# Kernel optimization log

Hardware: AMD Instinct MI355X
Metric: run time of the kernel (lower is better)

Reference implementation:

```python
import jax, jax.numpy as jnp
import numpy as np

B, T, SEQ = 8, 129, 128
H, N, NL, NE, V = 512, 64, 4, 128, 18

def _gelu(x):
    return jax.nn.gelu(x, approximate=False)

def _conv2d(x, w, b, stride):
    y = jax.lax.conv_general_dilated(x, w, (stride, stride), 'VALID',
                                     dimension_numbers=('NCHW', 'OIHW', 'NCHW'))
    return y + b[None, :, None, None]

def _layernorm(x, g, b, eps=1e-5):
    mu = jnp.mean(x, axis=-1, keepdims=True)
    var = jnp.mean(jnp.square(x - mu), axis=-1, keepdims=True)
    return (x - mu) * jax.lax.rsqrt(var + eps) * g + b

def _s4_kernel(log_dt, A_re, A_im, C_re, C_im, L):
    # Diagonal SSM (ZOH discretization, B=1): K[h,l] = 2*Re(sum_n Ceff * exp(dt*A)^l)
    dt = jnp.exp(log_dt)[:, None]                  # [H,1]
    A = A_re + 1j * A_im                            # [H,N] complex64
    dtA = (dt * A).astype(jnp.complex64)
    C = (C_re + 1j * C_im).astype(jnp.complex64)
    Ceff = C * (jnp.exp(dtA) - 1.0) / A             # [H,N]
    vand = jnp.exp(dtA[:, :, None] * jnp.arange(L, dtype=jnp.float32))  # [H,N,L]
    return 2.0 * jnp.einsum('hn,hnl->hl', Ceff, vand).real

def _fft_conv(u, K, D):
    # u: [B,H,L]  K: [H,L]  causal conv via zero-padded FFT
    L = u.shape[-1]
    n = 2 * L
    Uf = jnp.fft.rfft(u, n=n)
    Kf = jnp.fft.rfft(K, n=n)
    y = jnp.fft.irfft(Uf * Kf[None], n=n)[..., :L]
    return y + D[None, :, None] * u

def setup_inputs() -> dict:
    key = jax.random.key(0)
    ks = jax.random.split(key, 32)
    d = {}
    d['states'] = jax.random.uniform(ks[0], (B, T, 4, 84, 84), dtype=jnp.float32)
    d['actions'] = jax.random.randint(ks[1], (B, T), 0, V)
    d['rtgs'] = jax.random.uniform(ks[2], (B, T, 1), dtype=jnp.float32)
    s = 0.02
    d['enc_w1'] = jax.random.normal(ks[3], (32, 4, 8, 8)) * s
    d['enc_b1'] = jnp.zeros((32,))
    d['enc_w2'] = jax.random.normal(ks[4], (64, 32, 4, 4)) * s
    d['enc_b2'] = jnp.zeros((64,))
    d['enc_w3'] = jax.random.normal(ks[5], (64, 64, 3, 3)) * s
    d['enc_b3'] = jnp.zeros((64,))
    d['enc_lw'] = jax.random.normal(ks[6], (3136, NE)) * s
    d['enc_lb'] = jnp.zeros((NE,))
    d['ret_w'] = jax.random.normal(ks[7], (1, NE)) * s
    d['ret_b'] = jnp.zeros((NE,))
    d['act_emb'] = jax.random.normal(ks[8], (V, NE)) * s
    d['proj_w'] = jax.random.normal(ks[9], (3 * NE, H)) * s
    d['proj_b'] = jnp.zeros((H,))
    d['pre_w'] = jax.random.normal(ks[10], (H, H)) * s
    d['pre_b'] = jnp.zeros((H,))
    d['ln_g'] = jnp.ones((NL, H))
    d['ln_b'] = jnp.zeros((NL, H))
    lo, hi = np.log(1e-3), np.log(1e-1)
    d['log_dt'] = lo + jax.random.uniform(ks[11], (NL, H)) * (hi - lo)
    d['A_re'] = -0.5 * jnp.ones((NL, H, N))
    d['A_im'] = jnp.broadcast_to(np.pi * jnp.arange(N, dtype=jnp.float32), (NL, H, N)).copy()
    d['C_re'] = jax.random.normal(ks[12], (NL, H, N)) * (0.5 ** 0.5)
    d['C_im'] = jax.random.normal(ks[13], (NL, H, N)) * (0.5 ** 0.5)
    d['Dp'] = jax.random.normal(ks[14], (NL, H))
    d['aft_w'] = jax.random.normal(ks[15], (NL, H, H)) * s
    d['aft_b'] = jnp.zeros((NL, H))
    d['out_w'] = jax.random.normal(ks[16], (H, V)) * s
    return d

def reference(states, actions, rtgs, enc_w1, enc_b1, enc_w2, enc_b2, enc_w3, enc_b3,
              enc_lw, enc_lb, ret_w, ret_b, act_emb, proj_w, proj_b, pre_w, pre_b,
              ln_g, ln_b, log_dt, A_re, A_im, C_re, C_im, Dp, aft_w, aft_b, out_w):
    S = actions.shape[1] - 1  # del_r = 1
    # state encoder over B*S frames
    x = states[:, 1:].reshape(-1, 4, 84, 84)
    x = jax.nn.relu(_conv2d(x, enc_w1, enc_b1, 4))
    x = jax.nn.relu(_conv2d(x, enc_w2, enc_b2, 2))
    x = jax.nn.relu(_conv2d(x, enc_w3, enc_b3, 1))
    se = jnp.tanh(x.reshape(x.shape[0], -1) @ enc_lw + enc_lb)          # [B*S, NE]
    ae = jnp.tanh(act_emb[actions[:, :S].reshape(-1)])                   # [B*S, NE]
    re = jnp.tanh(rtgs[:, :S].reshape(-1, 1) @ ret_w + ret_b)            # [B*S, NE]
    u = jnp.concatenate([se, ae, re], axis=-1) @ proj_w + proj_b
    u = u.reshape(states.shape[0], S, H)
    y = _gelu(u) @ pre_w + pre_b                                          # beforeblock
    for i in range(NL):
        r = _layernorm(y, ln_g[i], ln_b[i])
        v = jnp.transpose(r, (0, 2, 1))                                   # [B,H,S]
        K = _s4_kernel(log_dt[i], A_re[i], A_im[i], C_re[i], C_im[i], S)
        c = _fft_conv(v, K, Dp[i])
        c = jnp.transpose(c, (0, 2, 1))                                   # [B,S,H]
        c = _gelu(_gelu(c) @ aft_w[i] + aft_b[i])
        y = c + y                                                          # s4_resnet
    logits = y @ out_w                                                     # [B,S,V]
    return logits
```

## Files before the change

kernel.cpp:

```cpp
#include <hip/hip_runtime.h>

#define Bq 8
#define Tq 129
#define Sq 128
#define Hq 512
#define Nq 64
#define NLq 4
#define NEq 128
#define Vq 18

typedef unsigned short u16;
typedef unsigned int u32;
typedef __attribute__((ext_vector_type(8))) short short8v;
typedef __attribute__((ext_vector_type(4))) float f32x4;

__device__ __forceinline__ float gelu_f(float x) {
  return 0.5f * x * (1.0f + erff(x * 0.70710678118654752f));
}

__device__ __forceinline__ u16 f2b(float x) {
  union { float f; unsigned int u; } v; v.f = x;
  unsigned int r = v.u + 0x7FFFu + ((v.u >> 16) & 1u);
  return (u16)(r >> 16);
}

__device__ __forceinline__ float b2f_lo(u32 u) {
  union { unsigned int u; float f; } v; v.u = u << 16; return v.f;
}
__device__ __forceinline__ float b2f_hi(u32 u) {
  union { unsigned int u; float f; } v; v.u = u & 0xffff0000u; return v.f;
}

__global__ __launch_bounds__(256) void prep_k(
    const float* __restrict__ enc_lw, const float* __restrict__ proj_w,
    const float* __restrict__ pre_w, const float* __restrict__ aft_w,
    const float* __restrict__ out_w,
    const float* __restrict__ w1, const float* __restrict__ w2,
    const float* __restrict__ w3,
    u16* __restrict__ Wt_enc, u16* __restrict__ Wt_proj, u16* __restrict__ Wt_pre,
    u16* __restrict__ Wt_aft, u16* __restrict__ Wt_out,
    u16* __restrict__ B1t, u16* __restrict__ B2t, u16* __restrict__ B3t) {
  __shared__ u16 T[64][65];
  int bid = blockIdx.x;
  if (bid >= 474) {
    int i = (bid - 474) * 256 + threadIdx.x;
    if (i < 8192) {
      int n = i >> 8, k = i & 255;
      int ic = k >> 6, ky = (k >> 3) & 7, kx = k & 7;
      B1t[i] = f2b(w1[((n * 4 + ic) * 8 + ky) * 8 + kx]);
    } else if (i < 8192 + 32768) {
      int j = i - 8192;
      int n = j >> 9, k = j & 511;
      int kyx = k >> 5, ic = k & 31, ky = kyx >> 2, kx = kyx & 3;
      B2t[j] = f2b(w2[((n * 32 + ic) * 4 + ky) * 4 + kx]);
    } else if (i < 8192 + 32768 + 36864) {
      int j = i - 40960;
      int n = j / 576, k = j - n * 576;
      int ic = k & 63, kyx = k >> 6, ky = kyx / 3, kx = kyx % 3;
      B3t[j] = f2b(w3[((n * 64 + ic) * 3 + ky) * 3 + kx]);
    }
    return;
  }
  const float* src; u16* dst; int K, N, kt, nt, t;
  if (bid < 98)       { t = bid;       src = enc_lw; dst = Wt_enc;  K = 3136; N = 128; kt = t >> 1; nt = t & 1; }
  else if (bid < 146) { t = bid - 98;  src = proj_w; dst = Wt_proj; K = 384;  N = 512; kt = t >> 3; nt = t & 7; }
  else if (bid < 210) { t = bid - 146; src = pre_w;  dst = Wt_pre;  K = 512;  N = 512; kt = t >> 3; nt = t & 7; }
  else if (bid < 466) { t = bid - 210; int L = t >> 6; t &= 63;
                        src = aft_w + (size_t)L * 262144; dst = Wt_aft + (size_t)L * 262144;
                        K = 512; N = 512; kt = t >> 3; nt = t & 7; }
  else                { t = bid - 466; src = out_w;  dst = Wt_out;  K = 512;  N = 18;  kt = t;      nt = 0; }
  int k0 = kt * 64, n0 = nt * 64;
  #pragma unroll
  for (int it = 0; it < 16; it++) {
    int idx = it * 256 + threadIdx.x;
    int rr = idx >> 6, cc = idx & 63;
    float v = (n0 + cc < N) ? src[(size_t)(k0 + rr) * N + n0 + cc] : 0.f;
    T[cc][rr] = f2b(v);
  }
  __syncthreads();
  #pragma unroll
  for (int it = 0; it < 16; it++) {
    int idx = it * 256 + threadIdx.x;
    int rr = idx >> 6, cc = idx & 63;
    dst[(size_t)(n0 + rr) * K + k0 + cc] = T[rr][cc];
  }
}

template<bool AF32, int EPI, bool STATS>
__global__ __launch_bounds__(256) void mgemm(const void* __restrict__ Av,
    const u16* __restrict__ Wt, const float* __restrict__ bias,
    const float* __restrict__ res, void* __restrict__ Cv,
    float2* __restrict__ part, int M, int K, int N, int ldc) {
  __shared__ u16 As[4][64][40];
  __shared__ u16 Bs[4][64][40];
  int tid = threadIdx.x;
  int bn = blockIdx.x * 64, bm = blockIdx.y * 64;
  int lane = tid & 63, w = tid >> 6;
  int q = lane >> 4, r = lane & 15;
  int wm = (w >> 1) * 32, wn = (w & 1) * 32;
  int am = tid >> 2, ak0 = (tid & 3) * 8;
  f32x4 acc[2][2] = {};
  for (int k0 = 0; k0 < K; k0 += 128) {
    #pragma unroll
    for (int st = 0; st < 4; st++) {
      int kk = k0 + st * 32 + ak0;
      if constexpr (AF32) {
        const float* A = (const float*)Av;
        const float* src = A + (size_t)(bm + am) * K + kk;
        float4 v0 = *(const float4*)src;
        float4 v1 = *(const float4*)(src + 4);
        ushort4 lo, hi;
        lo.x = f2b(v0.x); lo.y = f2b(v0.y); lo.z = f2b(v0.z); lo.w = f2b(v0.w);
        hi.x = f2b(v1.x); hi.y = f2b(v1.y); hi.z = f2b(v1.z); hi.w = f2b(v1.w);
        *(ushort4*)&As[st][am][ak0] = lo;
        *(ushort4*)&As[st][am][ak0 + 4] = hi;
      } else {
        *(short8v*)&As[st][am][ak0] =
            *(const short8v*)((const u16*)Av + (size_t)(bm + am) * K + kk);
      }
      *(short8v*)&Bs[st][am][ak0] = *(const short8v*)(Wt + (size_t)(bn + am) * K + kk);
    }
    __syncthreads();
    #pragma unroll
    for (int st = 0; st < 4; st++) {
      short8v a0 = *(const short8v*)&As[st][wm + r][q * 8];
      short8v a1 = *(const short8v*)&As[st][wm + 16 + r][q * 8];
      short8v b0 = *(const short8v*)&Bs[st][wn + r][q * 8];
      short8v b1 = *(const short8v*)&Bs[st][wn + 16 + r][q * 8];
      acc[0][0] = __builtin_amdgcn_mfma_f32_16x16x32_bf16(a0, b0, acc[0][0], 0, 0, 0);
      acc[0][1] = __builtin_amdgcn_mfma_f32_16x16x32_bf16(a0, b1, acc[0][1], 0, 0, 0);
      acc[1][0] = __builtin_amdgcn_mfma_f32_16x16x32_bf16(a1, b0, acc[1][0], 0, 0, 0);
      acc[1][1] = __builtin_amdgcn_mfma_f32_16x16x32_bf16(a1, b1, acc[1][1], 0, 0, 0);
    }
    __syncthreads();
  }
  float yv[2][2][4];
  #pragma unroll
  for (int ms = 0; ms < 2; ms++) {
    #pragma unroll
    for (int ns = 0; ns < 2; ns++) {
      #pragma unroll
      for (int reg = 0; reg < 4; reg++) {
        int m = bm + wm + ms * 16 + q * 4 + reg;
        int n = bn + wn + ns * 16 + r;
        if (n < N) {
          float v = acc[ms][ns][reg] + (bias ? bias[n] : 0.f);
          if (EPI == 0) { ((float*)Cv)[(size_t)m * ldc + n] = v; yv[ms][ns][reg] = v; }
          if (EPI == 2) ((u16*)Cv)[(size_t)m * ldc + n] = f2b(gelu_f(v));
          if (EPI == 3) {
            float o = gelu_f(v) + res[(size_t)m * ldc + n];
            ((float*)Cv)[(size_t)m * ldc + n] = o; yv[ms][ns][reg] = o;
          }
        }
      }
    }
  }
  if constexpr (STATS) {
    #pragma unroll
    for (int ms = 0; ms < 2; ms++) {
      #pragma unroll
      for (int reg = 0; reg < 4; reg++) {
        float s = yv[ms][0][reg] + yv[ms][1][reg];
        float s2 = yv[ms][0][reg] * yv[ms][0][reg] + yv[ms][1][reg] * yv[ms][1][reg];
        #pragma unroll
        for (int o = 1; o <= 8; o <<= 1) {
          s += __shfl_xor(s, o);
          s2 += __shfl_xor(s2, o);
        }
        if (r == 0) {
          int m = bm + wm + ms * 16 + q * 4 + reg;
          part[(size_t)(blockIdx.x * 2 + (w & 1)) * 1024 + m] = make_float2(s, s2);
        }
      }
    }
  }
}

__global__ __launch_bounds__(256) void enc_gemm(const u16* __restrict__ A,
    const u16* __restrict__ Wt, float* __restrict__ Cp) {
  __shared__ u16 As[64][40];
  __shared__ u16 Bs[64][40];
  int tid = threadIdx.x;
  int bn = blockIdx.x * 64, bm = blockIdx.y * 64, kc = blockIdx.z;
  int lane = tid & 63, w = tid >> 6;
  int q = lane >> 4, r = lane & 15;
  int wm = (w >> 1) * 32, wn = (w & 1) * 32;
  int am = tid >> 2, ak = (tid & 3) * 8;
  f32x4 acc[2][2] = {};
  int kend = kc * 448 + 448;
  for (int k0 = kc * 448; k0 < kend; k0 += 32) {
    *(short8v*)&As[am][ak] = *(const short8v*)(A + (size_t)(bm + am) * 3136 + k0 + ak);
    *(short8v*)&Bs[am][ak] = *(const short8v*)(Wt + (size_t)(bn + am) * 3136 + k0 + ak);
    __syncthreads();
    short8v a0 = *(const short8v*)&As[wm + r][q * 8];
    short8v a1 = *(const short8v*)&As[wm + 16 + r][q * 8];
    short8v b0 = *(const short8v*)&Bs[wn + r][q * 8];
    short8v b1 = *(const short8v*)&Bs[wn + 16 + r][q * 8];
    acc[0][0] = __builtin_amdgcn_mfma_f32_16x16x32_bf16(a0, b0, acc[0][0], 0, 0, 0);
    acc[0][1] = __builtin_amdgcn_mfma_f32_16x16x32_bf16(a0, b1, acc[0][1], 0, 0, 0);
    acc[1][0] = __builtin_amdgcn_mfma_f32_16x16x32_bf16(a1, b0, acc[1][0], 0, 0, 0);
    acc[1][1] = __builtin_amdgcn_mfma_f32_16x16x32_bf16(a1, b1, acc[1][1], 0, 0, 0);
    __syncthreads();
  }
  #pragma unroll
  for (int ms = 0; ms < 2; ms++)
    #pragma unroll
    for (int ns = 0; ns < 2; ns++)
      #pragma unroll
      for (int reg = 0; reg < 4; reg++) {
        int m = bm + wm + ms * 16 + q * 4 + reg;
        int n = bn + wn + ns * 16 + r;
        Cp[(size_t)(kc * 1024 + m) * 128 + n] = acc[ms][ns][reg];
      }
}

__global__ __launch_bounds__(256) void embedred_k(const float* __restrict__ Cp,
    const float* __restrict__ enc_lb, const int* __restrict__ actions,
    const float* __restrict__ rtgs, const float* __restrict__ act_emb,
    const float* __restrict__ ret_w, const float* __restrict__ ret_b,
    u16* __restrict__ uin) {
  int f = blockIdx.x;
  int b = f >> 7, s = f & 127;
  int e = threadIdx.x;
  if (e < 128) {
    float sum = enc_lb[e];
    #pragma unroll
    for (int kc = 0; kc < 7; kc++) sum += Cp[(size_t)(kc * 1024 + f) * 128 + e];
    uin[(size_t)f * 384 + e] = f2b(tanhf(sum));
    uin[(size_t)f * 384 + 256 + e] =
        f2b(tanhf(fmaf(rtgs[b * Tq + s], ret_w[e], ret_b[e])));
  } else {
    int ee = e - 128;
    int a = actions[b * Tq + s];
    uin[(size_t)f * 384 + 128 + ee] = f2b(tanhf(act_emb[a * NEq + ee]));
  }
}

__global__ __launch_bounds__(256) void conv1_mfma(const float* __restrict__ states,
    const u16* __restrict__ B1t, const float* __restrict__ bias, u16* __restrict__ out) {
  __shared__ u16 lds[4][3696];
  int blk = blockIdx.x;
  int fr = blk >> 1, half = blk & 1;
  int b = fr >> 7, s = fr & 127;
  const float* in = states + (size_t)(b * Tq + s + 1) * 28224 + half * 3360;
  int tid = threadIdx.x;
  #pragma unroll
  for (int it = 0; it < 15; it++) {
    int idx = tid + it * 256;
    if (idx < 3696) {
      int ic = idx >> 2; ic = idx / 924;
      int r2 = idx - ic * 924;
      float4 v = *(const float4*)(in + ic * 7056 + r2 * 4);
      ushort4 uv;
      uv.x = f2b(v.x); uv.y = f2b(v.y); uv.z = f2b(v.z); uv.w = f2b(v.w);
      *(ushort4*)&lds[ic][r2 * 4] = uv;
    }
  }
  int lane = tid & 63, w = tid >> 6;
  int q = lane >> 4, r = lane & 15;
  short8v bfr[2][8];
  #pragma unroll
  for (int nt = 0; nt < 2; nt++)
    #pragma unroll
    for (int ks = 0; ks < 8; ks++)
      bfr[nt][ks] = *(const short8v*)(B1t + (nt * 16 + r) * 256 + ks * 32 + q * 8);
  __syncthreads();
  for (int mt = w; mt < 13; mt += 4) {
    int m = mt * 16 + r; if (m > 199) m = 199;
    int oyl = m / 20, ox = m % 20;
    f32x4 acc0 = {0.f, 0.f, 0.f, 0.f}, acc1 = {0.f, 0.f, 0.f, 0.f};
    #pragma unroll
    for (int ks = 0; ks < 8; ks++) {
      int k0 = ks * 32 + q * 8;
      int ic = k0 >> 6, ky = (k0 >> 3) & 7;
      int ai = (oyl * 4 + ky) * 84 + ox * 4;
      ushort4 lo = *(const ushort4*)&lds[ic][ai];
      ushort4 hi = *(const ushort4*)&lds[ic][ai + 4];
      short8v av;
      av[0] = (short)lo.x; av[1] = (short)lo.y; av[2] = (short)lo.z; av[3] = (short)lo.w;
      av[4] = (short)hi.x; av[5] = (short)hi.y; av[6] = (short)hi.z; av[7] = (short)hi.w;
      acc0 = __builtin_amdgcn_mfma_f32_16x16x32_bf16(av, bfr[0][ks], acc0, 0, 0, 0);
      acc1 = __builtin_amdgcn_mfma_f32_16x16x32_bf16(av, bfr[1][ks], acc1, 0, 0, 0);
    }
    #pragma unroll
    for (int reg = 0; reg < 4; reg++) {
      int pos = mt * 16 + q * 4 + reg;
      if (pos < 200) {
        int gp = half * 200 + pos;
        out[(size_t)fr * 12800 + gp * 32 + r]      = f2b(fmaxf(acc0[reg] + bias[r], 0.f));
        out[(size_t)fr * 12800 + gp * 32 + 16 + r] = f2b(fmaxf(acc1[reg] + bias[16 + r], 0.f));
      }
    }
  }
}

__global__ __launch_bounds__(256) void conv2_mfma(const u16* __restrict__ in_,
    const u16* __restrict__ B2t, const float* __restrict__ bias, u16* __restrict__ out) {
  __shared__ u16 lds[12800];
  int fr = blockIdx.x;
  int tid = threadIdx.x;
  const short8v* src = (const short8v*)(in_ + (size_t)fr * 12800);
  short8v* dst = (short8v*)lds;
  #pragma unroll
  for (int it = 0; it < 7; it++) {
    int idx = tid + it * 256;
    if (idx < 1600) dst[idx] = src[idx];
  }
  int lane = tid & 63, w = tid >> 6;
  int q = lane >> 4, r = lane & 15;
  int n = w * 16 + r;
  short8v bfr[16];
  #pragma unroll
  for (int ks = 0; ks < 16; ks++)
    bfr[ks] = *(const short8v*)(B2t + n * 512 + ks * 32 + q * 8);
  __syncthreads();
  float bn = bias[n];
  #pragma unroll
  for (int mt = 0; mt < 6; mt++) {
    int m = mt * 16 + r; if (m > 80) m = 80;
    int oy = m / 9, ox = m % 9;
    f32x4 acc = {0.f, 0.f, 0.f, 0.f};
    #pragma unroll
    for (int ks = 0; ks < 16; ks++) {
      int ky = ks >> 2, kx = ks & 3;
      int ai = ((oy * 2 + ky) * 20 + ox * 2 + kx) * 32 + q * 8;
      short8v av = *(const short8v*)&lds[ai];
      acc = __builtin_amdgcn_mfma_f32_16x16x32_bf16(av, bfr[ks], acc, 0, 0, 0);
    }
    #pragma unroll
    for (int reg = 0; reg < 4; reg++) {
      int pos = mt * 16 + q * 4 + reg;
      if (pos < 81)
        out[(size_t)fr * 5184 + pos * 64 + n] = f2b(fmaxf(acc[reg] + bn, 0.f));
    }
  }
}

__global__ __launch_bounds__(256) void conv3_mfma(const u16* __restrict__ in_,
    const u16* __restrict__ B3t, const float* __restrict__ bias, u16* __restrict__ out) {
  __shared__ u16 lds[5184];
  int fr = blockIdx.x;
  int tid = threadIdx.x;
  const short8v* src = (const short8v*)(in_ + (size_t)fr * 5184);
  short8v* dst = (short8v*)lds;
  #pragma unroll
  for (int it = 0; it < 3; it++) {
    int idx = tid + it * 256;
    if (idx < 648) dst[idx] = src[idx];
  }
  int lane = tid & 63, w = tid >> 6;
  int q = lane >> 4, r = lane & 15;
  int n = w * 16 + r;
  short8v bfr[18];
  #pragma unroll
  for (int ks = 0; ks < 18; ks++)
    bfr[ks] = *(const short8v*)(B3t + n * 576 + ks * 32 + q * 8);
  __syncthreads();
  float bn = bias[n];
  #pragma unroll
  for (int mt = 0; mt < 4; mt++) {
    int m = mt * 16 + r; if (m > 48) m = 48;
    int oy = m / 7, ox = m % 7;
    f32x4 acc = {0.f, 0.f, 0.f, 0.f};
    #pragma unroll
    for (int ks = 0; ks < 18; ks++) {
      int kyx = ks >> 1;
      int ky = kyx / 3, kx = kyx % 3;
      int ic0 = (ks & 1) * 32 + q * 8;
      int ai = ((oy + ky) * 9 + ox + kx) * 64 + ic0;
      short8v av = *(const short8v*)&lds[ai];
      acc = __builtin_amdgcn_mfma_f32_16x16x32_bf16(av, bfr[ks], acc, 0, 0, 0);
    }
    #pragma unroll
    for (int reg = 0; reg < 4; reg++) {
      int pos = mt * 16 + q * 4 + reg;
      if (pos < 49)
        out[(size_t)fr * 3136 + n * 49 + pos] = f2b(fmaxf(acc[reg] + bn, 0.f));
    }
  }
}

__global__ __launch_bounds__(64) void s4k_gen(const float* __restrict__ log_dt,
    const float* __restrict__ A_re, const float* __restrict__ A_im,
    const float* __restrict__ C_re, const float* __restrict__ C_im,
    u16* __restrict__ Ktb) {
  __shared__ float con[64][129];
  int lh = blockIdx.x;
  int n = threadIdx.x;
  float dt = expf(log_dt[lh]);
  float ar = A_re[(size_t)lh * Nq + n], ai = A_im[(size_t)lh * Nq + n];
  float al = dt * ar, be = dt * ai;
  float er = expf(al);
  float wr = er * cosf(be), wi = er * sinf(be);
  float zr = wr - 1.0f, zi = wi;
  float den = 1.0f / (ar * ar + ai * ai);
  float tr = (zr * ar + zi * ai) * den, ti = (zi * ar - zr * ai) * den;
  float Cr = C_re[(size_t)lh * Nq + n], Ci = C_im[(size_t)lh * Nq + n];
  float cr = Cr * tr - Ci * ti, ci = Cr * ti + Ci * tr;
  float curr = 1.0f, curi = 0.0f;
  for (int l = 0; l < Sq; l++) {
    con[n][l] = cr * curr - ci * curi;
    float nr = curr * wr - curi * wi;
    curi = curr * wi + curi * wr;
    curr = nr;
  }
  __syncthreads();
  int layer = lh >> 9, h = lh & 511;
  #pragma unroll
  for (int li = n; li < Sq; li += 64) {
    float s = 0.f;
    for (int j = 0; j < 64; j++) s += con[j][li];
    Ktb[((size_t)layer * Sq + li) * Hq + h] = f2b(2.0f * s);
  }
}

__global__ __launch_bounds__(256) void sconv_fused(const float* __restrict__ y,
    const float2* __restrict__ part, const float* __restrict__ g,
    const float* __restrict__ bta, const u16* __restrict__ Kt,
    const float* __restrict__ D, u16* __restrict__ cact) {
  __shared__ u32 P[16][140];
  __shared__ u32 KL[16][132];
  __shared__ float2 statl[128];
  int hc = blockIdx.x, b = blockIdx.y;
  int t = threadIdx.x;
  int h0 = hc * 32;
  if (t < 128) {
    float s = 0.f, s2 = 0.f;
    #pragma unroll
    for (int pc = 0; pc < 16; pc++) {
      float2 pp = part[(size_t)pc * 1024 + b * Sq + t];
      s += pp.x; s2 += pp.y;
    }
    float mu = s * (1.f / Hq);
    float var = s2 * (1.f / Hq) - mu * mu;
    statl[t] = make_float2(mu, rsqrtf(var + 1e-5f));
  }
  if (t < 16) {
    #pragma unroll
    for (int i = 0; i < 8; i++) P[t][i] = 0;
  }
  #pragma unroll
  for (int it = 0; it < 8; it++) {
    int idx = it * 256 + t;
    int p = idx & 15, j = idx >> 4;
    KL[p][j] = *(const u32*)(Kt + (size_t)j * Hq + h0 + 2 * p);
  }
  __syncthreads();
  #pragma unroll
  for (int it = 0; it < 8; it++) {
    int idx = it * 256 + t;
    int p = idx & 15, s = idx >> 4;
    int row = b * Sq + s;
    float2 v = *(const float2*)(y + (size_t)row * Hq + h0 + 2 * p);
    float2 st = statl[s];
    float2 gg = *(const float2*)(g + h0 + 2 * p);
    float2 bb = *(const float2*)(bta + h0 + 2 * p);
    float r0 = (v.x - st.x) * st.y * gg.x + bb.x;
    float r1 = (v.y - st.x) * st.y * gg.y + bb.y;
    P[p][8 + s] = (u32)f2b(r0) | ((u32)f2b(r1) << 16);
  }
  __syncthreads();
  int p = t & 15, sg = t >> 4;
  int s0 = sg * 8;
  float acc0[8], acc1[8];
  float2 d2 = *(const float2*)(D + h0 + 2 * p);
  #pragma unroll
  for (int k = 0; k < 8; k++) {
    u32 rv = P[p][8 + s0 + k];
    acc0[k] = d2.x * b2f_lo(rv);
    acc1[k] = d2.y * b2f_hi(rv);
  }
  for (int jb = 0; jb <= sg; jb++) {
    int base = (sg - jb) * 8;
    u32 wv[16], kv[8];
    *(uint4*)&wv[0]  = *(const uint4*)&P[p][base];
    *(uint4*)&wv[4]  = *(const uint4*)&P[p][base + 4];
    *(uint4*)&wv[8]  = *(const uint4*)&P[p][base + 8];
    *(uint4*)&wv[12] = *(const uint4*)&P[p][base + 12];
    *(uint4*)&kv[0]  = *(const uint4*)&KL[p][jb * 8];
    *(uint4*)&kv[4]  = *(const uint4*)&KL[p][jb * 8 + 4];
    float wlo[16], whi[16], klo[8], khi[8];
    #pragma unroll
    for (int i = 0; i < 16; i++) { wlo[i] = b2f_lo(wv[i]); whi[i] = b2f_hi(wv[i]); }
    #pragma unroll
    for (int i = 0; i < 8; i++) { klo[i] = b2f_lo(kv[i]); khi[i] = b2f_hi(kv[i]); }
    #pragma unroll
    for (int jo = 0; jo < 8; jo++)
      #pragma unroll
      for (int k = 0; k < 8; k++) {
        acc0[k] = fmaf(klo[jo], wlo[8 + k - jo], acc0[k]);
        acc1[k] = fmaf(khi[jo], whi[8 + k - jo], acc1[k]);
      }
  }
  #pragma unroll
  for (int k = 0; k < 8; k++) {
    int s = s0 + k;
    u32 outv = (u32)f2b(gelu_f(acc0[k])) | ((u32)f2b(gelu_f(acc1[k])) << 16);
    *(u32*)(cact + ((size_t)(b * Sq + s)) * Hq + h0 + 2 * p) = outv;
  }
}

extern "C" void kernel_launch(void* const* d_in, const int* in_sizes, int n_in,
                              void* d_out, int out_size, void* d_ws, size_t ws_size,
                              hipStream_t stream) {
  const float* states  = (const float*)d_in[0];
  const int*   actions = (const int*)  d_in[1];
  const float* rtgs    = (const float*)d_in[2];
  const float* enc_w1  = (const float*)d_in[3];
  const float* enc_b1  = (const float*)d_in[4];
  const float* enc_w2  = (const float*)d_in[5];
  const float* enc_b2  = (const float*)d_in[6];
  const float* enc_w3  = (const float*)d_in[7];
  const float* enc_b3  = (const float*)d_in[8];
  const float* enc_lw  = (const float*)d_in[9];
  const float* enc_lb  = (const float*)d_in[10];
  const float* ret_w   = (const float*)d_in[11];
  const float* ret_b   = (const float*)d_in[12];
  const float* act_emb = (const float*)d_in[13];
  const float* proj_w  = (const float*)d_in[14];
  const float* proj_b  = (const float*)d_in[15];
  const float* pre_w   = (const float*)d_in[16];
  const float* pre_b   = (const float*)d_in[17];
  const float* ln_g    = (const float*)d_in[18];
  const float* ln_b    = (const float*)d_in[19];
  const float* log_dt  = (const float*)d_in[20];
  const float* A_re    = (const float*)d_in[21];
  const float* A_im    = (const float*)d_in[22];
  const float* C_re    = (const float*)d_in[23];
  const float* C_im    = (const float*)d_in[24];
  const float* Dp      = (const float*)d_in[25];
  const float* aft_w   = (const float*)d_in[26];
  const float* aft_b   = (const float*)d_in[27];
  const float* out_w   = (const float*)d_in[28];

  u16* Wt_enc  = (u16*)d_ws;
  u16* Wt_proj = Wt_enc + 401408;
  u16* Wt_pre  = Wt_proj + 196608;
  u16* Wt_aft  = Wt_pre + 262144;
  u16* Wt_out  = Wt_aft + 1048576;
  u16* B1t = Wt_out + 32768;
  u16* B2t = B1t + 8192;
  u16* B3t = B2t + 32768;
  u16* o1  = B3t + 36864;
  u16* o2  = o1 + 13107200;
  u16* x3b = o2 + 5308416;
  u16* uin = x3b + 3211264;
  u16* uact = uin + 393216;
  u16* cact = uact + 524288;
  u16* Ktb  = cact + 524288;
  float* y    = (float*)(Ktb + 262144);
  float* Cp   = y + 524288;
  float2* part = (float2*)(Cp + 917504);

  prep_k<<<778, 256, 0, stream>>>(enc_lw, proj_w, pre_w, aft_w, out_w,
                                  enc_w1, enc_w2, enc_w3,
                                  Wt_enc, Wt_proj, Wt_pre, Wt_aft, Wt_out,
                                  B1t, B2t, B3t);
  conv1_mfma<<<2048, 256, 0, stream>>>(states, B1t, enc_b1, o1);
  conv2_mfma<<<1024, 256, 0, stream>>>(o1, B2t, enc_b2, o2);
  conv3_mfma<<<1024, 256, 0, stream>>>(o2, B3t, enc_b3, x3b);
  enc_gemm<<<dim3(2, 16, 7), 256, 0, stream>>>(x3b, Wt_enc, Cp);
  embedred_k<<<1024, 256, 0, stream>>>(Cp, enc_lb, actions, rtgs, act_emb,
                                       ret_w, ret_b, uin);
  mgemm<false, 2, false><<<dim3(8, 16), 256, 0, stream>>>(uin, Wt_proj, proj_b,
      nullptr, uact, nullptr, 1024, 384, 512, 512);
  mgemm<false, 0, true><<<dim3(8, 16), 256, 0, stream>>>(uact, Wt_pre, pre_b,
      nullptr, y, part, 1024, 512, 512, 512);
  s4k_gen<<<2048, 64, 0, stream>>>(log_dt, A_re, A_im, C_re, C_im, Ktb);

  for (int i = 0; i < NLq; i++) {
    sconv_fused<<<dim3(16, 8), 256, 0, stream>>>(y, part, ln_g + i * Hq,
                                                 ln_b + i * Hq,
                                                 Ktb + (size_t)i * Sq * Hq,
                                                 Dp + i * Hq, cact);
    mgemm<false, 3, true><<<dim3(8, 16), 256, 0, stream>>>(cact,
        Wt_aft + (size_t)i * Hq * Hq, aft_b + i * Hq, y, y, part,
        1024, 512, 512, 512);
  }
  mgemm<true, 0, false><<<dim3(1, 16), 256, 0, stream>>>(y, Wt_out, nullptr,
      nullptr, (float*)d_out, nullptr, 1024, 512, Vq, Vq);
}
```

Baseline: 235.8 us.

## Split state conversion from conv1 and fuse conv2 with conv3

Input frames are now converted from fp32 to bf16 in a separate pass into a padded workspace buffer. conv1 then stages that buffer into LDS with direct global-to-LDS loads. conv2 and conv3 are merged into one kernel that keeps the conv2 output in LDS, so that intermediate no longer makes a round trip through global memory and one launch disappears. The price is an extra full write and re-read of the converted frames, roughly 67 MB each way, which could outweigh what the fusion saves.

```diff
diff --git a/kernel.cpp b/kernel.cpp
--- a/kernel.cpp
+++ b/kernel.cpp
@@ -29,6 +29,12 @@
 }
 __device__ __forceinline__ float b2f_hi(u32 u) {
   union { unsigned int u; float f; } v; v.u = u & 0xffff0000u; return v.f;
+}
+
+__device__ __forceinline__ void gload_lds16(const u16* gsrc, u16* ldst) {
+  __builtin_amdgcn_global_load_lds(
+      (const __attribute__((address_space(1))) unsigned int*)gsrc,
+      (__attribute__((address_space(3))) unsigned int*)ldst, 16, 0, 0);
 }
 
 __global__ __launch_bounds__(256) void prep_k(
@@ -86,6 +92,157 @@
   }
 }
 
+__global__ __launch_bounds__(256) void convert_k(const float* __restrict__ states,
+    u16* __restrict__ x1b) {
+  int blk = blockIdx.x;
+  int fr = blk >> 1, half = blk & 1;
+  int b = fr >> 7, s = fr & 127;
+  const float* src = states + (size_t)(b * Tq + s + 1) * 28224 + half * 3360;
+  u16* dst = x1b + (size_t)blk * 16384;
+  int tid = threadIdx.x;
+  #pragma unroll
+  for (int it = 0; it < 8; it++) {
+    int unit = it * 256 + tid;
+    if (unit < 1848) {
+      int ic = unit / 462;
+      int r2 = unit - ic * 462;
+      const float* sp = src + ic * 7056 + r2 * 8;
+      float4 v0 = *(const float4*)sp;
+      float4 v1 = *(const float4*)(sp + 4);
+      ushort4 a, c;
+      a.x = f2b(v0.x); a.y = f2b(v0.y); a.z = f2b(v0.z); a.w = f2b(v0.w);
+      c.x = f2b(v1.x); c.y = f2b(v1.y); c.z = f2b(v1.z); c.w = f2b(v1.w);
+      *(ushort4*)(dst + (size_t)unit * 8) = a;
+      *(ushort4*)(dst + (size_t)unit * 8 + 4) = c;
+    }
+  }
+}
+
+__global__ __launch_bounds__(256) void conv1_mfma(const u16* __restrict__ x1b,
+    const u16* __restrict__ B1t, const float* __restrict__ bias, u16* __restrict__ out) {
+  __shared__ u16 lds[16384];
+  int blk = blockIdx.x;
+  int fr = blk >> 1, half = blk & 1;
+  const u16* src = x1b + (size_t)blk * 16384;
+  int tid = threadIdx.x;
+  int wb = tid & 192;
+  #pragma unroll
+  for (int it = 0; it < 8; it++) {
+    int unit = it * 256 + tid;
+    gload_lds16(src + (size_t)unit * 8, &lds[(it * 256 + wb) * 8]);
+  }
+  int lane = tid & 63, w = tid >> 6;
+  int q = lane >> 4, r = lane & 15;
+  short8v bfr[2][8];
+  #pragma unroll
+  for (int nt = 0; nt < 2; nt++)
+    #pragma unroll
+    for (int ks = 0; ks < 8; ks++)
+      bfr[nt][ks] = *(const short8v*)(B1t + (nt * 16 + r) * 256 + ks * 32 + q * 8);
+  __syncthreads();
+  for (int mt = w; mt < 13; mt += 4) {
+    int m = mt * 16 + r; if (m > 199) m = 199;
+    int oyl = m / 20, ox = m % 20;
+    f32x4 acc0 = {0.f, 0.f, 0.f, 0.f}, acc1 = {0.f, 0.f, 0.f, 0.f};
+    #pragma unroll
+    for (int ks = 0; ks < 8; ks++) {
+      int k0 = ks * 32 + q * 8;
+      int ic = k0 >> 6, ky = (k0 >> 3) & 7;
+      int ai = ic * 3696 + (oyl * 4 + ky) * 84 + ox * 4;
+      ushort4 lo = *(const ushort4*)&lds[ai];
+      ushort4 hi = *(const ushort4*)&lds[ai + 4];
+      short8v av;
+      av[0] = (short)lo.x; av[1] = (short)lo.y; av[2] = (short)lo.z; av[3] = (short)lo.w;
+      av[4] = (short)hi.x; av[5] = (short)hi.y; av[6] = (short)hi.z; av[7] = (short)hi.w;
+      acc0 = __builtin_amdgcn_mfma_f32_16x16x32_bf16(av, bfr[0][ks], acc0, 0, 0, 0);
+      acc1 = __builtin_amdgcn_mfma_f32_16x16x32_bf16(av, bfr[1][ks], acc1, 0, 0, 0);
+    }
+    #pragma unroll
+    for (int reg = 0; reg < 4; reg++) {
+      int pos = mt * 16 + q * 4 + reg;
+      if (pos < 200) {
+        int gp = half * 200 + pos;
+        out[(size_t)fr * 12800 + gp * 32 + r]      = f2b(fmaxf(acc0[reg] + bias[r], 0.f));
+        out[(size_t)fr * 12800 + gp * 32 + 16 + r] = f2b(fmaxf(acc1[reg] + bias[16 + r], 0.f));
+      }
+    }
+  }
+}
+
+__global__ __launch_bounds__(256) void conv23_mfma(const u16* __restrict__ o1,
+    const u16* __restrict__ B2t, const u16* __restrict__ B3t,
+    const float* __restrict__ b2, const float* __restrict__ b3,
+    u16* __restrict__ x3b) {
+  __shared__ u16 o1l[12800];
+  __shared__ u16 o2l[5184];
+  int fr = blockIdx.x;
+  int tid = threadIdx.x;
+  int wb = tid & 192;
+  const u16* src = o1 + (size_t)fr * 12800;
+  #pragma unroll
+  for (int it = 0; it < 7; it++) {
+    if (it < 6 || tid < 64) {
+      int unit = it * 256 + tid;
+      gload_lds16(src + (size_t)unit * 8, &o1l[(it * 256 + wb) * 8]);
+    }
+  }
+  int lane = tid & 63, w = tid >> 6;
+  int q = lane >> 4, r = lane & 15;
+  int n = w * 16 + r;
+  short8v bfr2[16];
+  #pragma unroll
+  for (int ks = 0; ks < 16; ks++)
+    bfr2[ks] = *(const short8v*)(B2t + n * 512 + ks * 32 + q * 8);
+  __syncthreads();
+  float bn2 = b2[n];
+  #pragma unroll
+  for (int mt = 0; mt < 6; mt++) {
+    int m = mt * 16 + r; if (m > 80) m = 80;
+    int oy = m / 9, ox = m % 9;
+    f32x4 acc = {0.f, 0.f, 0.f, 0.f};
+    #pragma unroll
+    for (int ks = 0; ks < 16; ks++) {
+      int ky = ks >> 2, kx = ks & 3;
+      int ai = ((oy * 2 + ky) * 20 + ox * 2 + kx) * 32 + q * 8;
+      short8v av = *(const short8v*)&o1l[ai];
+      acc = __builtin_amdgcn_mfma_f32_16x16x32_bf16(av, bfr2[ks], acc, 0, 0, 0);
+    }
+    #pragma unroll
+    for (int reg = 0; reg < 4; reg++) {
+      int pos = mt * 16 + q * 4 + reg;
+      if (pos < 81)
+        o2l[pos * 64 + n] = f2b(fmaxf(acc[reg] + bn2, 0.f));
+    }
+  }
+  short8v bfr3[18];
+  #pragma unroll
+  for (int ks = 0; ks < 18; ks++)
+    bfr3[ks] = *(const short8v*)(B3t + n * 576 + ks * 32 + q * 8);
+  __syncthreads();
+  float bn3 = b3[n];
+  #pragma unroll
+  for (int mt = 0; mt < 4; mt++) {
+    int m = mt * 16 + r; if (m > 48) m = 48;
+    int oy = m / 7, ox = m % 7;
+    f32x4 acc = {0.f, 0.f, 0.f, 0.f};
+    #pragma unroll
+    for (int ks = 0; ks < 18; ks++) {
+      int kyx = ks >> 1;
+      int ky = kyx / 3, kx = kyx % 3;
+      int ic0 = (ks & 1) * 32 + q * 8;
+      int ai = ((oy + ky) * 9 + ox + kx) * 64 + ic0;
+      short8v av = *(const short8v*)&o2l[ai];
+      acc = __builtin_amdgcn_mfma_f32_16x16x32_bf16(av, bfr3[ks], acc, 0, 0, 0);
+    }
+    #pragma unroll
+    for (int reg = 0; reg < 4; reg++) {
+      int pos = mt * 16 + q * 4 + reg;
+      if (pos < 49)
+        x3b[(size_t)fr * 3136 + n * 49 + pos] = f2b(fmaxf(acc[reg] + bn3, 0.f));
+    }
+  }
+}
+
 template<bool AF32, int EPI, bool STATS>
 __global__ __launch_bounds__(256) void mgemm(const void* __restrict__ Av,
     const u16* __restrict__ Wt, const float* __restrict__ bias,
@@ -233,150 +390,6 @@
     int ee = e - 128;
     int a = actions[b * Tq + s];
     uin[(size_t)f * 384 + 128 + ee] = f2b(tanhf(act_emb[a * NEq + ee]));
-  }
-}
-
-__global__ __launch_bounds__(256) void conv1_mfma(const float* __restrict__ states,
-    const u16* __restrict__ B1t, const float* __restrict__ bias, u16* __restrict__ out) {
-  __shared__ u16 lds[4][3696];
-  int blk = blockIdx.x;
-  int fr = blk >> 1, half = blk & 1;
-  int b = fr >> 7, s = fr & 127;
-  const float* in = states + (size_t)(b * Tq + s + 1) * 28224 + half * 3360;
-  int tid = threadIdx.x;
-  #pragma unroll
-  for (int it = 0; it < 15; it++) {
-    int idx = tid + it * 256;
-    if (idx < 3696) {
-      int ic = idx >> 2; ic = idx / 924;
-      int r2 = idx - ic * 924;
-      float4 v = *(const float4*)(in + ic * 7056 + r2 * 4);
-      ushort4 uv;
-      uv.x = f2b(v.x); uv.y = f2b(v.y); uv.z = f2b(v.z); uv.w = f2b(v.w);
-      *(ushort4*)&lds[ic][r2 * 4] = uv;
-    }
-  }
-  int lane = tid & 63, w = tid >> 6;
-  int q = lane >> 4, r = lane & 15;
-  short8v bfr[2][8];
-  #pragma unroll
-  for (int nt = 0; nt < 2; nt++)
-    #pragma unroll
-    for (int ks = 0; ks < 8; ks++)
-      bfr[nt][ks] = *(const short8v*)(B1t + (nt * 16 + r) * 256 + ks * 32 + q * 8);
-  __syncthreads();
-  for (int mt = w; mt < 13; mt += 4) {
-    int m = mt * 16 + r; if (m > 199) m = 199;
-    int oyl = m / 20, ox = m % 20;
-    f32x4 acc0 = {0.f, 0.f, 0.f, 0.f}, acc1 = {0.f, 0.f, 0.f, 0.f};
-    #pragma unroll
-    for (int ks = 0; ks < 8; ks++) {
-      int k0 = ks * 32 + q * 8;
-      int ic = k0 >> 6, ky = (k0 >> 3) & 7;
-      int ai = (oyl * 4 + ky) * 84 + ox * 4;
-      ushort4 lo = *(const ushort4*)&lds[ic][ai];
-      ushort4 hi = *(const ushort4*)&lds[ic][ai + 4];
-      short8v av;
-      av[0] = (short)lo.x; av[1] = (short)lo.y; av[2] = (short)lo.z; av[3] = (short)lo.w;
-      av[4] = (short)hi.x; av[5] = (short)hi.y; av[6] = (short)hi.z; av[7] = (short)hi.w;
-      acc0 = __builtin_amdgcn_mfma_f32_16x16x32_bf16(av, bfr[0][ks], acc0, 0, 0, 0);
-      acc1 = __builtin_amdgcn_mfma_f32_16x16x32_bf16(av, bfr[1][ks], acc1, 0, 0, 0);
-    }
-    #pragma unroll
-    for (int reg = 0; reg < 4; reg++) {
-      int pos = mt * 16 + q * 4 + reg;
-      if (pos < 200) {
-        int gp = half * 200 + pos;
-        out[(size_t)fr * 12800 + gp * 32 + r]      = f2b(fmaxf(acc0[reg] + bias[r], 0.f));
-        out[(size_t)fr * 12800 + gp * 32 + 16 + r] = f2b(fmaxf(acc1[reg] + bias[16 + r], 0.f));
-      }
-    }
-  }
-}
-
-__global__ __launch_bounds__(256) void conv2_mfma(const u16* __restrict__ in_,
-    const u16* __restrict__ B2t, const float* __restrict__ bias, u16* __restrict__ out) {
-  __shared__ u16 lds[12800];
-  int fr = blockIdx.x;
-  int tid = threadIdx.x;
-  const short8v* src = (const short8v*)(in_ + (size_t)fr * 12800);
-  short8v* dst = (short8v*)lds;
-  #pragma unroll
-  for (int it = 0; it < 7; it++) {
-    int idx = tid + it * 256;
-    if (idx < 1600) dst[idx] = src[idx];
-  }
-  int lane = tid & 63, w = tid >> 6;
-  int q = lane >> 4, r = lane & 15;
-  int n = w * 16 + r;
-  short8v bfr[16];
-  #pragma unroll
-  for (int ks = 0; ks < 16; ks++)
-    bfr[ks] = *(const short8v*)(B2t + n * 512 + ks * 32 + q * 8);
-  __syncthreads();
-  float bn = bias[n];
-  #pragma unroll
-  for (int mt = 0; mt < 6; mt++) {
-    int m = mt * 16 + r; if (m > 80) m = 80;
-    int oy = m / 9, ox = m % 9;
-    f32x4 acc = {0.f, 0.f, 0.f, 0.f};
-    #pragma unroll
-    for (int ks = 0; ks < 16; ks++) {
-      int ky = ks >> 2, kx = ks & 3;
-      int ai = ((oy * 2 + ky) * 20 + ox * 2 + kx) * 32 + q * 8;
-      short8v av = *(const short8v*)&lds[ai];
-      acc = __builtin_amdgcn_mfma_f32_16x16x32_bf16(av, bfr[ks], acc, 0, 0, 0);
-    }
-    #pragma unroll
-    for (int reg = 0; reg < 4; reg++) {
-      int pos = mt * 16 + q * 4 + reg;
-      if (pos < 81)
-        out[(size_t)fr * 5184 + pos * 64 + n] = f2b(fmaxf(acc[reg] + bn, 0.f));
-    }
-  }
-}
-
-__global__ __launch_bounds__(256) void conv3_mfma(const u16* __restrict__ in_,
-    const u16* __restrict__ B3t, const float* __restrict__ bias, u16* __restrict__ out) {
-  __shared__ u16 lds[5184];
-  int fr = blockIdx.x;
-  int tid = threadIdx.x;
-  const short8v* src = (const short8v*)(in_ + (size_t)fr * 5184);
-  short8v* dst = (short8v*)lds;
-  #pragma unroll
-  for (int it = 0; it < 3; it++) {
-    int idx = tid + it * 256;
-    if (idx < 648) dst[idx] = src[idx];
-  }
-  int lane = tid & 63, w = tid >> 6;
-  int q = lane >> 4, r = lane & 15;
-  int n = w * 16 + r;
-  short8v bfr[18];
-  #pragma unroll
-  for (int ks = 0; ks < 18; ks++)
-    bfr[ks] = *(const short8v*)(B3t + n * 576 + ks * 32 + q * 8);
-  __syncthreads();
-  float bn = bias[n];
-  #pragma unroll
-  for (int mt = 0; mt < 4; mt++) {
-    int m = mt * 16 + r; if (m > 48) m = 48;
-    int oy = m / 7, ox = m % 7;
-    f32x4 acc = {0.f, 0.f, 0.f, 0.f};
-    #pragma unroll
-    for (int ks = 0; ks < 18; ks++) {
-      int kyx = ks >> 1;
-      int ky = kyx / 3, kx = kyx % 3;
-      int ic0 = (ks & 1) * 32 + q * 8;
-      int ai = ((oy + ky) * 9 + ox + kx) * 64 + ic0;
-      short8v av = *(const short8v*)&lds[ai];
-      acc = __builtin_amdgcn_mfma_f32_16x16x32_bf16(av, bfr[ks], acc, 0, 0, 0);
-    }
-    #pragma unroll
-    for (int reg = 0; reg < 4; reg++) {
-      int pos = mt * 16 + q * 4 + reg;
-      if (pos < 49)
-        out[(size_t)fr * 3136 + n * 49 + pos] = f2b(fmaxf(acc[reg] + bn, 0.f));
-    }
   }
 }
 
@@ -541,9 +554,9 @@
   u16* B1t = Wt_out + 32768;
   u16* B2t = B1t + 8192;
   u16* B3t = B2t + 32768;
-  u16* o1  = B3t + 36864;
-  u16* o2  = o1 + 13107200;
-  u16* x3b = o2 + 5308416;
+  u16* x1b = B3t + 36864;
+  u16* o1  = x1b + 33554432;
+  u16* x3b = o1 + 13107200;
   u16* uin = x3b + 3211264;
   u16* uact = uin + 393216;
   u16* cact = uact + 524288;
@@ -556,9 +569,9 @@
                                   enc_w1, enc_w2, enc_w3,
                                   Wt_enc, Wt_proj, Wt_pre, Wt_aft, Wt_out,
                                   B1t, B2t, B3t);
-  conv1_mfma<<<2048, 256, 0, stream>>>(states, B1t, enc_b1, o1);
-  conv2_mfma<<<1024, 256, 0, stream>>>(o1, B2t, enc_b2, o2);
-  conv3_mfma<<<1024, 256, 0, stream>>>(o2, B3t, enc_b3, x3b);
+  convert_k<<<2048, 256, 0, stream>>>(states, x1b);
+  conv1_mfma<<<2048, 256, 0, stream>>>(x1b, B1t, enc_b1, o1);
+  conv23_mfma<<<1024, 256, 0, stream>>>(o1, B2t, B3t, enc_b2, enc_b3, x3b);
   enc_gemm<<<dim3(2, 16, 7), 256, 0, stream>>>(x3b, Wt_enc, Cp);
   embedred_k<<<1024, 256, 0, stream>>>(Cp, enc_lb, actions, rtgs, act_emb,
                                        ret_w, ret_b, uin);
```

Result: slower. 246.8 us (+4.7%).
